# Performance work log

Hardware: AMD Instinct MI355X
Metric: run time of the kernel (lower is better)

## Reference

```python
import jax, jax.numpy as jnp
import numpy as np

B, H, W, C = 32, 64, 64, 192
WS, SHIFT, NH = 8, 4, 6
HID = int(C * 2.0)
N = WS * WS
HD = C // NH
SCALE = HD ** -0.5


def _rel_index():
    coords = np.stack(np.meshgrid(np.arange(WS), np.arange(WS), indexing='ij')).reshape(2, -1)
    rel = (coords[:, :, None] - coords[:, None, :]).transpose(1, 2, 0)
    rel[:, :, 0] += WS - 1
    rel[:, :, 1] += WS - 1
    rel[:, :, 0] *= 2 * WS - 1
    return rel.sum(-1)  # [N, N] int


def _attn_mask():
    img = np.zeros((H, W))
    cnt = 0
    sl = (slice(0, -WS), slice(-WS, -SHIFT), slice(-SHIFT, None))
    for hs in sl:
        for ws_ in sl:
            img[hs, ws_] = cnt
            cnt += 1
    mw = img.reshape(H // WS, WS, W // WS, WS).transpose(0, 2, 1, 3).reshape(-1, N)
    am = mw[:, None, :] - mw[:, :, None]  # unsqueeze(1) - unsqueeze(2)
    return np.where(am != 0, -100.0, 0.0).astype(np.float32)  # [nW, N, N]

REL_IDX = jnp.asarray(_rel_index())
ATTN_MASK = jnp.asarray(_attn_mask())


def _ln(x, g, b, eps=1e-5):
    m = jnp.mean(x, -1, keepdims=True)
    v = jnp.mean((x - m) ** 2, -1, keepdims=True)
    return (x - m) * jax.lax.rsqrt(v + eps) * g + b


def setup_inputs() -> dict:
    key = jax.random.key(0)
    ks = jax.random.split(key, 16)
    s = 0.02
    return {
        'x': jax.random.normal(ks[0], (B, H, W, C), jnp.float32),
        'norm1_g': jnp.ones((C,), jnp.float32),
        'norm1_b': jnp.zeros((C,), jnp.float32),
        'qkv_w': jax.random.normal(ks[1], (C, 3 * C), jnp.float32) * s,
        'qkv_b': jnp.zeros((3 * C,), jnp.float32),
        'proj_w': jax.random.normal(ks[2], (C, C), jnp.float32) * s,
        'proj_b': jnp.zeros((C,), jnp.float32),
        'rel_bias_table': jax.random.normal(ks[3], ((2 * WS - 1) ** 2, NH), jnp.float32) * s,
        'norm2_g': jnp.ones((C,), jnp.float32),
        'norm2_b': jnp.zeros((C,), jnp.float32),
        'mlp_w1': jax.random.normal(ks[4], (C, HID), jnp.float32) * s,
        'mlp_b1': jnp.zeros((HID,), jnp.float32),
        'mlp_w2': jax.random.normal(ks[5], (HID, C), jnp.float32) * s,
        'mlp_b2': jnp.zeros((C,), jnp.float32),
    }


def reference(x, norm1_g, norm1_b, qkv_w, qkv_b, proj_w, proj_b, rel_bias_table,
              norm2_g, norm2_b, mlp_w1, mlp_b1, mlp_w2, mlp_b2):
    nWh, nWw = H // WS, W // WS
    nW = nWh * nWw
    shortcut = x
    h = _ln(x, norm1_g, norm1_b)
    # cyclic shift
    h = jnp.roll(h, shift=(-SHIFT, -SHIFT), axis=(1, 2))
    # window partition -> [B*nW, N, C]
    hw = h.reshape(B, nWh, WS, nWw, WS, C).transpose(0, 1, 3, 2, 4, 5).reshape(B * nW, N, C)
    # qkv
    qkv = hw @ qkv_w + qkv_b  # [B_, N, 3C]
    qkv = qkv.reshape(B * nW, N, 3, NH, HD).transpose(2, 0, 3, 1, 4)
    q, k, v = qkv[0], qkv[1], qkv[2]  # [B_, NH, N, HD]
    attn = jnp.einsum('bhnd,bhmd->bhnm', q * SCALE, k)
    # relative position bias: [NH, N, N]
    bias = rel_bias_table[REL_IDX.reshape(-1)].reshape(N, N, NH).transpose(2, 0, 1)
    attn = attn + bias[None]
    # shift mask
    attn = attn.reshape(B, nW, NH, N, N) + ATTN_MASK[None, :, None]
    attn = jax.nn.softmax(attn.reshape(B * nW, NH, N, N), axis=-1)
    out = jnp.einsum('bhnm,bhmd->bhnd', attn, v).transpose(0, 2, 1, 3).reshape(B * nW, N, C)
    out = out @ proj_w + proj_b
    # window reverse
    out = out.reshape(B, nWh, nWw, WS, WS, C).transpose(0, 1, 3, 2, 4, 5).reshape(B, H, W, C)
    out = jnp.roll(out, shift=(SHIFT, SHIFT), axis=(1, 2))
    h = shortcut + out
    # MLP
    m = _ln(h, norm2_g, norm2_b)
    m = jax.nn.gelu(m @ mlp_w1 + mlp_b1, approximate=False) @ mlp_w2 + mlp_b2
    return h + m
```

## Files before the change

### kernel.cpp

```cpp
#include <hip/hip_runtime.h>
#include <hip/hip_bf16.h>

#define CC 192

typedef __attribute__((ext_vector_type(8))) short bf16x8;
typedef __attribute__((ext_vector_type(4))) float f32x4;

__device__ __forceinline__ unsigned short f2bf(float f) {
    unsigned int u = __float_as_uint(f);
    u = (u + 0x7fffu + ((u >> 16) & 1u)) >> 16;
    return (unsigned short)u;
}

__device__ __forceinline__ float bf2f(unsigned short u) {
    return __uint_as_float(((unsigned int)u) << 16);
}

__device__ __forceinline__ float fast_exp2(float x) {
#if __has_builtin(__builtin_amdgcn_exp2f)
    return __builtin_amdgcn_exp2f(x);
#else
    return __expf(0.69314718055994531f * x);
#endif
}

__device__ __forceinline__ f32x4 mfma16(bf16x8 a, bf16x8 b, f32x4 c) {
    return __builtin_amdgcn_mfma_f32_16x16x32_bf16(a, b, c, 0, 0, 0);
}

__global__ void k_prep(const float* __restrict__ qkv_w, const float* __restrict__ proj_w,
                       const float* __restrict__ w1, const float* __restrict__ w2,
                       const float* __restrict__ relTab,
                       unsigned short* __restrict__ qkvT, unsigned short* __restrict__ projT,
                       unsigned short* __restrict__ w1T, unsigned short* __restrict__ w2T,
                       unsigned short* __restrict__ biasT4) {
    int idx = blockIdx.x * blockDim.x + threadIdx.x;
    if (idx < 110592) { int n = idx / 192, k = idx % 192; qkvT[idx] = f2bf(qkv_w[k * 576 + n]); return; }
    idx -= 110592;
    if (idx < 36864)  { int n = idx / 192, k = idx % 192; projT[idx] = f2bf(proj_w[k * 192 + n]); return; }
    idx -= 36864;
    if (idx < 73728)  { int n = idx / 192, k = idx % 192; w1T[idx] = f2bf(w1[k * 384 + n]); return; }
    idx -= 73728;
    if (idx < 73728)  { int n = idx / 384, k = idx % 384; w2T[idx] = f2bf(w2[k * 192 + n]); return; }
    idx -= 73728;
    if (idx < 98304) {
        const int cls = idx / 24576, rem = idx % 24576;
        const int h = rem >> 12, i = (rem >> 6) & 63, j = rem & 63;
        const int yi = i >> 3, xi = i & 7, yj = j >> 3, xj = j & 7;
        const int rel = (yi - yj + 7) * 15 + (xi - xj + 7);
        float v = relTab[rel * 6 + h];
        const int bH = cls >> 1, bW = cls & 1;
        const int idi = (bH ? (yi >= 4 ? 2 : 1) : 0) * 3 + (bW ? (xi >= 4 ? 2 : 1) : 0);
        const int idj = (bH ? (yj >= 4 ? 2 : 1) : 0) * 3 + (bW ? (xj >= 4 ? 2 : 1) : 0);
        if (idi != idj) v -= 100.f;
        biasT4[idx] = f2bf(v * 1.4426950408889634f);
    }
}

__global__ __launch_bounds__(768, 3) void k_fused(
    const float* __restrict__ x,
    const float* __restrict__ n1g, const float* __restrict__ n1b,
    const unsigned short* __restrict__ qkvT, const float* __restrict__ qkv_b,
    const unsigned short* __restrict__ projT, const float* __restrict__ proj_b,
    const unsigned short* __restrict__ biasT4,
    const float* __restrict__ n2g, const float* __restrict__ n2b,
    const unsigned short* __restrict__ w1T, const float* __restrict__ b1,
    const unsigned short* __restrict__ w2T, const float* __restrict__ b2,
    float* __restrict__ out)
{
    __shared__ __align__(16) char smem[73728];
    __shared__ int sOpos[64];
    char* const rA = smem;
    char* const rQ = smem + 24576;
    char* const rK = smem + 49152;

    const int tid = threadIdx.x;
    const int wid = blockIdx.x;
    const int b = wid >> 6;
    const int win = wid & 63;
    const int wh = win >> 3, ww = win & 7;
    const int lane = tid & 63;
    const int wave = tid >> 6;
    const int lhi = lane >> 4, llo = lane & 15;

    if (tid < 512) {
        const int tok = tid >> 3;
        const int ch0 = (tid & 7) * 24;
        const int yi = tok >> 3, xi = tok & 7;
        const int oy = (wh * 8 + yi + 4) & 63;
        const int ox = (ww * 8 + xi + 4) & 63;
        const int base = ((b * 64 + oy) * 64 + ox) * CC;
        if ((tid & 7) == 0) sOpos[tok] = base;
        float v[24];
        float s = 0.f, ss = 0.f;
        #pragma unroll
        for (int i = 0; i < 6; ++i) {
            const float4 f = *(const float4*)(x + base + ch0 + i * 4);
            v[i*4+0]=f.x; v[i*4+1]=f.y; v[i*4+2]=f.z; v[i*4+3]=f.w;
            s  += f.x + f.y + f.z + f.w;
            ss += f.x*f.x + f.y*f.y + f.z*f.z + f.w*f.w;
        }
        s  += __shfl_xor(s, 1);  s  += __shfl_xor(s, 2);  s  += __shfl_xor(s, 4);
        ss += __shfl_xor(ss, 1); ss += __shfl_xor(ss, 2); ss += __shfl_xor(ss, 4);
        const float mean = s * (1.f / 192.f);
        const float rstd = rsqrtf(ss * (1.f / 192.f) - mean * mean + 1e-5f);
        char* aBase = rA + tok * 384;
        const int sw = (tok & 7) << 4;
        #pragma unroll
        for (int i = 0; i < 12; ++i) {
            const int c = ch0 + i * 2;
            const float a0 = (v[i*2+0] - mean) * rstd * n1g[c]   + n1b[c];
            const float a1 = (v[i*2+1] - mean) * rstd * n1g[c+1] + n1b[c+1];
            *(unsigned int*)(aBase + ((c * 2) ^ sw)) =
                (unsigned int)f2bf(a0) | ((unsigned int)f2bf(a1) << 16);
        }
    }
    __syncthreads();

    {
        const int cbase = wave * 48;
        f32x4 acc[4][3] = {};
        #pragma unroll
        for (int ks = 0; ks < 6; ++ks) {
            bf16x8 af[4];
            const int kbyte = ks * 64 + lhi * 16;
            #pragma unroll
            for (int m = 0; m < 4; ++m) {
                const int row = m * 16 + llo;
                af[m] = *(const bf16x8*)(rA + row * 384 + (kbyte ^ ((row & 7) << 4)));
            }
            #pragma unroll
            for (int n = 0; n < 3; ++n) {
                const int col = cbase + n * 16 + llo;
                const bf16x8 bfr = *(const bf16x8*)(qkvT + col * 192 + ks * 32 + lhi * 8);
                #pragma unroll
                for (int m = 0; m < 4; ++m) acc[m][n] = mfma16(af[m], bfr, acc[m][n]);
            }
        }
        __syncthreads();
        #pragma unroll
        for (int n = 0; n < 3; ++n) {
            const int c0 = cbase + n * 16;
            const int which = c0 / 192;
            const int rem = c0 - which * 192;
            const int h = rem >> 5;
            const int d = (rem & 31) + llo;
            const float bia = qkv_b[c0 + llo];
            #pragma unroll
            for (int m = 0; m < 4; ++m) {
                #pragma unroll
                for (int r = 0; r < 4; ++r) {
                    const int row = m * 16 + lhi * 4 + r;
                    if (which == 0)
                        *(unsigned short*)(rQ + h * 4096 + row * 64 + ((2 * d) ^ ((row & 3) << 4)))
                            = f2bf((acc[m][n][r] + bia) * 0.2550510257216822f);
                    else if (which == 1)
                        *(unsigned short*)(rK + h * 4096 + row * 64 + ((2 * d) ^ ((row & 3) << 4)))
                            = f2bf(acc[m][n][r] + bia);
                    else
                        *(unsigned short*)(rA + h * 4096 + d * 128 + ((2 * row) ^ ((d & 7) << 4)))
                            = f2bf(acc[m][n][r] + bia);
                }
            }
        }
    }
    __syncthreads();

    const int h = wave >> 1;
    const int mh = wave & 1;
    f32x4 pacc[2][2] = {};
    float rinv[2][4];
    {
        bf16x8 qf[2], kf[4];
        #pragma unroll
        for (int m = 0; m < 2; ++m) {
            const int t = (mh * 2 + m) * 16 + llo;
            qf[m] = *(const bf16x8*)(rQ + h * 4096 + t * 64 + ((lhi * 16) ^ ((t & 3) << 4)));
        }
        #pragma unroll
        for (int n = 0; n < 4; ++n) {
            const int t = n * 16 + llo;
            kf[n] = *(const bf16x8*)(rK + h * 4096 + t * 64 + ((lhi * 16) ^ ((t & 3) << 4)));
        }
        __syncthreads();

        f32x4 sacc[2][4] = {};
        #pragma unroll
        for (int m = 0; m < 2; ++m)
            #pragma unroll
            for (int n = 0; n < 4; ++n)
                sacc[m][n] = mfma16(qf[m], kf[n], sacc[m][n]);

        const int cls = ((wh == 7) ? 2 : 0) + ((ww == 7) ? 1 : 0);
        const unsigned short* bT = biasT4 + cls * 24576 + h * 4096;
        #pragma unroll
        for (int m = 0; m < 2; ++m) {
            #pragma unroll
            for (int r = 0; r < 4; ++r) {
                const int i = (mh * 2 + m) * 16 + lhi * 4 + r;
                float sum = 0.f;
                unsigned short pb[4];
                #pragma unroll
                for (int n = 0; n < 4; ++n) {
                    const int j = n * 16 + llo;
                    const float e = fast_exp2(sacc[m][n][r] + bf2f(bT[i * 64 + j]));
                    sum += e;
                    pb[n] = f2bf(e);
                }
                sum += __shfl_xor(sum, 1);
                sum += __shfl_xor(sum, 2);
                sum += __shfl_xor(sum, 4);
                sum += __shfl_xor(sum, 8);
                rinv[m][r] = 1.f / sum;
                #pragma unroll
                for (int n = 0; n < 4; ++n) {
                    const int j = n * 16 + llo;
                    *(unsigned short*)(rQ + h * 8192 + i * 128 + ((2 * j) ^ ((i & 7) << 4))) = pb[n];
                }
            }
        }
        #pragma unroll
        for (int ks = 0; ks < 2; ++ks) {
            bf16x8 pf[2];
            #pragma unroll
            for (int m = 0; m < 2; ++m) {
                const int t = (mh * 2 + m) * 16 + llo;
                pf[m] = *(const bf16x8*)(rQ + h * 8192 + t * 128 + ((ks * 64 + lhi * 16) ^ ((t & 7) << 4)));
            }
            #pragma unroll
            for (int n = 0; n < 2; ++n) {
                const int d = n * 16 + llo;
                const bf16x8 vf = *(const bf16x8*)(rA + h * 4096 + d * 128 + ((ks * 64 + lhi * 16) ^ ((d & 7) << 4)));
                #pragma unroll
                for (int m = 0; m < 2; ++m) pacc[m][n] = mfma16(pf[m], vf, pacc[m][n]);
            }
        }
    }
    __syncthreads();
    {
        #pragma unroll
        for (int m = 0; m < 2; ++m) {
            #pragma unroll
            for (int n = 0; n < 2; ++n) {
                const int c = h * 32 + n * 16 + llo;
                #pragma unroll
                for (int r = 0; r < 4; ++r) {
                    const int i = (mh * 2 + m) * 16 + lhi * 4 + r;
                    *(unsigned short*)(rA + i * 384 + ((c * 2) ^ ((i & 7) << 4)))
                        = f2bf(pacc[m][n][r] * rinv[m][r]);
                }
            }
        }
    }
    __syncthreads();

    {
        const int cbase = wave * 16;
        f32x4 acc[4] = {};
        #pragma unroll
        for (int ks = 0; ks < 6; ++ks) {
            bf16x8 af[4];
            const int kbyte = ks * 64 + lhi * 16;
            #pragma unroll
            for (int m = 0; m < 4; ++m) {
                const int row = m * 16 + llo;
                af[m] = *(const bf16x8*)(rA + row * 384 + (kbyte ^ ((row & 7) << 4)));
            }
            const int col = cbase + llo;
            const bf16x8 bfr = *(const bf16x8*)(projT + col * 192 + ks * 32 + lhi * 8);
            #pragma unroll
            for (int m = 0; m < 4; ++m) acc[m] = mfma16(af[m], bfr, acc[m]);
        }
        const int c = cbase + llo;
        const float pb = proj_b[c];
        #pragma unroll
        for (int m = 0; m < 4; ++m) {
            #pragma unroll
            for (int r = 0; r < 4; ++r) {
                const int i = m * 16 + lhi * 4 + r;
                const float hv = x[sOpos[i] + c] + acc[m][r] + pb;
                *(unsigned short*)(rQ + i * 384 + ((2 * c) ^ ((i & 7) << 4))) = f2bf(hv);
            }
        }
    }
    __syncthreads();

    if (tid < 512) {
        const int tok = tid >> 3;
        const int ch0 = (tid & 7) * 24;
        const int sw = (tok & 7) << 4;
        float v[24]; float s = 0.f, ss = 0.f;
        #pragma unroll
        for (int i = 0; i < 12; ++i) {
            const int c = ch0 + i * 2;
            const unsigned uu = *(const unsigned*)(rQ + tok * 384 + ((2 * c) ^ sw));
            const float a0 = bf2f((unsigned short)uu);
            const float a1 = bf2f((unsigned short)(uu >> 16));
            v[2*i] = a0; v[2*i+1] = a1;
            s += a0 + a1;
            ss += a0 * a0 + a1 * a1;
        }
        s  += __shfl_xor(s, 1);  s  += __shfl_xor(s, 2);  s  += __shfl_xor(s, 4);
        ss += __shfl_xor(ss, 1); ss += __shfl_xor(ss, 2); ss += __shfl_xor(ss, 4);
        const float mean = s * (1.f / 192.f);
        const float rstd = rsqrtf(ss * (1.f / 192.f) - mean * mean + 1e-5f);
        char* aBase = rA + tok * 384;
        #pragma unroll
        for (int i = 0; i < 12; ++i) {
            const int c = ch0 + i * 2;
            const float a0 = (v[i*2]   - mean) * rstd * n2g[c]   + n2b[c];
            const float a1 = (v[i*2+1] - mean) * rstd * n2g[c+1] + n2b[c+1];
            *(unsigned int*)(aBase + ((c * 2) ^ sw)) =
                (unsigned int)f2bf(a0) | ((unsigned int)f2bf(a1) << 16);
        }
    }
    __syncthreads();

    f32x4 accM[4] = {};
    #pragma unroll
    for (int hh = 0; hh < 2; ++hh) {
        {
            f32x4 a1[4] = {};
            #pragma unroll
            for (int ks = 0; ks < 6; ++ks) {
                bf16x8 af[4];
                const int kbyte = ks * 64 + lhi * 16;
                #pragma unroll
                for (int m = 0; m < 4; ++m) {
                    const int row = m * 16 + llo;
                    af[m] = *(const bf16x8*)(rA + row * 384 + (kbyte ^ ((row & 7) << 4)));
                }
                const bf16x8 bfr = *(const bf16x8*)(w1T + (hh * 192 + wave * 16 + llo) * 192 + ks * 32 + lhi * 8);
                #pragma unroll
                for (int m = 0; m < 4; ++m) a1[m] = mfma16(af[m], bfr, a1[m]);
            }
            const int cl = wave * 16 + llo;
            const float bb = b1[hh * 192 + cl];
            #pragma unroll
            for (int m = 0; m < 4; ++m) {
                #pragma unroll
                for (int r = 0; r < 4; ++r) {
                    const int i = m * 16 + lhi * 4 + r;
                    const float u = a1[m][r] + bb;
                    const float xx = 2.3022211096534824f * (u + 0.044715f * u * u * u);
                    const float g = u / (1.f + fast_exp2(-xx));
                    *(unsigned short*)(rK + i * 384 + ((2 * cl) ^ ((i & 7) << 4))) = f2bf(g);
                }
            }
        }
        __syncthreads();
        {
            #pragma unroll
            for (int ks = 0; ks < 6; ++ks) {
                bf16x8 af[4];
                const int kbyte = ks * 64 + lhi * 16;
                #pragma unroll
                for (int m = 0; m < 4; ++m) {
                    const int row = m * 16 + llo;
                    af[m] = *(const bf16x8*)(rK + row * 384 + (kbyte ^ ((row & 7) << 4)));
                }
                const bf16x8 bfr = *(const bf16x8*)(w2T + (wave * 16 + llo) * 384 + hh * 192 + ks * 32 + lhi * 8);
                #pragma unroll
                for (int m = 0; m < 4; ++m) accM[m] = mfma16(af[m], bfr, accM[m]);
            }
        }
        if (hh == 0) __syncthreads();
    }
    {
        const int c = wave * 16 + llo;
        const float bb = b2[c];
        #pragma unroll
        for (int m = 0; m < 4; ++m) {
            #pragma unroll
            for (int r = 0; r < 4; ++r) {
                const int i = m * 16 + lhi * 4 + r;
                const float hv = bf2f(*(const unsigned short*)(rQ + i * 384 + ((2 * c) ^ ((i & 7) << 4))));
                out[sOpos[i] + c] = hv + accM[m][r] + bb;
            }
        }
    }
}

extern "C" void kernel_launch(void* const* d_in, const int* in_sizes, int n_in,
                              void* d_out, int out_size, void* d_ws, size_t ws_size,
                              hipStream_t stream)
{
    const float* x      = (const float*)d_in[0];
    const float* n1g    = (const float*)d_in[1];
    const float* n1b    = (const float*)d_in[2];
    const float* qkv_w  = (const float*)d_in[3];
    const float* qkv_b  = (const float*)d_in[4];
    const float* proj_w = (const float*)d_in[5];
    const float* proj_b = (const float*)d_in[6];
    const float* relTab = (const float*)d_in[7];
    const float* n2g    = (const float*)d_in[8];
    const float* n2b    = (const float*)d_in[9];
    const float* w1     = (const float*)d_in[10];
    const float* b1     = (const float*)d_in[11];
    const float* w2     = (const float*)d_in[12];
    const float* b2     = (const float*)d_in[13];
    float* out = (float*)d_out;

    char* ws = (char*)d_ws;
    unsigned short* qkvT   = (unsigned short*)(ws);
    unsigned short* projT  = (unsigned short*)(ws + 221184);
    unsigned short* w1T    = (unsigned short*)(ws + 294912);
    unsigned short* w2T    = (unsigned short*)(ws + 442368);
    unsigned short* biasT4 = (unsigned short*)(ws + 589824);

    k_prep<<<1536, 256, 0, stream>>>(qkv_w, proj_w, w1, w2, relTab, qkvT, projT, w1T, w2T, biasT4);
    k_fused<<<2048, 768, 0, stream>>>(x, n1g, n1b, qkvT, qkv_b, projT, proj_b, biasT4,
                                      n2g, n2b, w1T, b1, w2T, b2, out);
}
```

Baseline: 277.2 us.

## Use dedicated LDS buffer for P and full MLP hidden to drop barriers

Adds a separate 48KB LDS region so attention probabilities no longer overwrite the Q buffer, which lets one __syncthreads after the Q/K fragment loads be removed. The MLP is restructured so the full 384-wide hidden activation is computed in one pass (each wave now does 32 columns), stored in LDS, then the second GEMM runs over all 12 k-steps with one barrier instead of two half-passes. The bf16 conversion switches to the HIP intrinsic. LDS per block grows from about 72KB to 120KB, which may lower how many 768-thread blocks fit per CU below the launch_bounds target of 3.

Result: no change. 275.0 us (-0.8%).

```diff
diff --git a/kernel.cpp b/kernel.cpp
--- a/kernel.cpp
+++ b/kernel.cpp
@@ -7,9 +7,10 @@
 typedef __attribute__((ext_vector_type(4))) float f32x4;
 
 __device__ __forceinline__ unsigned short f2bf(float f) {
-    unsigned int u = __float_as_uint(f);
-    u = (u + 0x7fffu + ((u >> 16) & 1u)) >> 16;
-    return (unsigned short)u;
+    __hip_bfloat16 h = __float2bfloat16(f);
+    unsigned short u;
+    __builtin_memcpy(&u, &h, 2);
+    return u;
 }
 
 __device__ __forceinline__ float bf2f(unsigned short u) {
@@ -68,11 +69,12 @@
     const unsigned short* __restrict__ w2T, const float* __restrict__ b2,
     float* __restrict__ out)
 {
-    __shared__ __align__(16) char smem[73728];
+    __shared__ __align__(16) char smem[122880];
     __shared__ int sOpos[64];
     char* const rA = smem;
     char* const rQ = smem + 24576;
     char* const rK = smem + 49152;
+    char* const rP = smem + 73728;
 
     const int tid = threadIdx.x;
     const int wid = blockIdx.x;
@@ -131,8 +133,7 @@
             }
             #pragma unroll
             for (int n = 0; n < 3; ++n) {
-                const int col = cbase + n * 16 + llo;
-                const bf16x8 bfr = *(const bf16x8*)(qkvT + col * 192 + ks * 32 + lhi * 8);
+                const bf16x8 bfr = *(const bf16x8*)(qkvT + (cbase + n * 16 + llo) * 192 + ks * 32 + lhi * 8);
                 #pragma unroll
                 for (int m = 0; m < 4; ++m) acc[m][n] = mfma16(af[m], bfr, acc[m][n]);
             }
@@ -182,7 +183,6 @@
             const int t = n * 16 + llo;
             kf[n] = *(const bf16x8*)(rK + h * 4096 + t * 64 + ((lhi * 16) ^ ((t & 3) << 4)));
         }
-        __syncthreads();
 
         f32x4 sacc[2][4] = {};
         #pragma unroll
@@ -193,6 +193,7 @@
 
         const int cls = ((wh == 7) ? 2 : 0) + ((ww == 7) ? 1 : 0);
         const unsigned short* bT = biasT4 + cls * 24576 + h * 4096;
+        char* const pBase = rP + h * 8192;
         #pragma unroll
         for (int m = 0; m < 2; ++m) {
             #pragma unroll
@@ -215,7 +216,7 @@
                 #pragma unroll
                 for (int n = 0; n < 4; ++n) {
                     const int j = n * 16 + llo;
-                    *(unsigned short*)(rQ + h * 8192 + i * 128 + ((2 * j) ^ ((i & 7) << 4))) = pb[n];
+                    *(unsigned short*)(pBase + i * 128 + ((2 * j) ^ ((i & 7) << 4))) = pb[n];
                 }
             }
         }
@@ -225,7 +226,7 @@
             #pragma unroll
             for (int m = 0; m < 2; ++m) {
                 const int t = (mh * 2 + m) * 16 + llo;
-                pf[m] = *(const bf16x8*)(rQ + h * 8192 + t * 128 + ((ks * 64 + lhi * 16) ^ ((t & 7) << 4)));
+                pf[m] = *(const bf16x8*)(pBase + t * 128 + ((ks * 64 + lhi * 16) ^ ((t & 7) << 4)));
             }
             #pragma unroll
             for (int n = 0; n < 2; ++n) {
@@ -266,8 +267,7 @@
                 const int row = m * 16 + llo;
                 af[m] = *(const bf16x8*)(rA + row * 384 + (kbyte ^ ((row & 7) << 4)));
             }
-            const int col = cbase + llo;
-            const bf16x8 bfr = *(const bf16x8*)(projT + col * 192 + ks * 32 + lhi * 8);
+            const bf16x8 bfr = *(const bf16x8*)(projT + (cbase + llo) * 192 + ks * 32 + lhi * 8);
             #pragma unroll
             for (int m = 0; m < 4; ++m) acc[m] = mfma16(af[m], bfr, acc[m]);
         }
@@ -316,58 +316,60 @@
     }
     __syncthreads();
 
-    f32x4 accM[4] = {};
-    #pragma unroll
-    for (int hh = 0; hh < 2; ++hh) {
-        {
-            f32x4 a1[4] = {};
-            #pragma unroll
-            for (int ks = 0; ks < 6; ++ks) {
-                bf16x8 af[4];
-                const int kbyte = ks * 64 + lhi * 16;
-                #pragma unroll
-                for (int m = 0; m < 4; ++m) {
-                    const int row = m * 16 + llo;
-                    af[m] = *(const bf16x8*)(rA + row * 384 + (kbyte ^ ((row & 7) << 4)));
-                }
-                const bf16x8 bfr = *(const bf16x8*)(w1T + (hh * 192 + wave * 16 + llo) * 192 + ks * 32 + lhi * 8);
-                #pragma unroll
-                for (int m = 0; m < 4; ++m) a1[m] = mfma16(af[m], bfr, a1[m]);
-            }
-            const int cl = wave * 16 + llo;
-            const float bb = b1[hh * 192 + cl];
+    {
+        const int cbase = wave * 32;
+        f32x4 a1[4][2] = {};
+        #pragma unroll
+        for (int ks = 0; ks < 6; ++ks) {
+            bf16x8 af[4];
+            const int kbyte = ks * 64 + lhi * 16;
+            #pragma unroll
+            for (int m = 0; m < 4; ++m) {
+                const int row = m * 16 + llo;
+                af[m] = *(const bf16x8*)(rA + row * 384 + (kbyte ^ ((row & 7) << 4)));
+            }
+            #pragma unroll
+            for (int n = 0; n < 2; ++n) {
+                const bf16x8 bfr = *(const bf16x8*)(w1T + (cbase + n * 16 + llo) * 192 + ks * 32 + lhi * 8);
+                #pragma unroll
+                for (int m = 0; m < 4; ++m) a1[m][n] = mfma16(af[m], bfr, a1[m][n]);
+            }
+        }
+        #pragma unroll
+        for (int n = 0; n < 2; ++n) {
+            const int c = cbase + n * 16 + llo;
+            const float bb = b1[c];
             #pragma unroll
             for (int m = 0; m < 4; ++m) {
                 #pragma unroll
                 for (int r = 0; r < 4; ++r) {
                     const int i = m * 16 + lhi * 4 + r;
-                    const float u = a1[m][r] + bb;
+                    const float u = a1[m][n][r] + bb;
                     const float xx = 2.3022211096534824f * (u + 0.044715f * u * u * u);
                     const float g = u / (1.f + fast_exp2(-xx));
-                    *(unsigned short*)(rK + i * 384 + ((2 * cl) ^ ((i & 7) << 4))) = f2bf(g);
+                    *(unsigned short*)(rP + i * 768 + ((2 * c) ^ ((i & 7) << 4))) = f2bf(g);
                 }
             }
         }
-        __syncthreads();
-        {
-            #pragma unroll
-            for (int ks = 0; ks < 6; ++ks) {
-                bf16x8 af[4];
-                const int kbyte = ks * 64 + lhi * 16;
-                #pragma unroll
-                for (int m = 0; m < 4; ++m) {
-                    const int row = m * 16 + llo;
-                    af[m] = *(const bf16x8*)(rK + row * 384 + (kbyte ^ ((row & 7) << 4)));
-                }
-                const bf16x8 bfr = *(const bf16x8*)(w2T + (wave * 16 + llo) * 384 + hh * 192 + ks * 32 + lhi * 8);
-                #pragma unroll
-                for (int m = 0; m < 4; ++m) accM[m] = mfma16(af[m], bfr, accM[m]);
-            }
-        }
-        if (hh == 0) __syncthreads();
-    }
+    }
+    __syncthreads();
+
     {
         const int c = wave * 16 + llo;
+        f32x4 accM[4] = {};
+        #pragma unroll
+        for (int ks = 0; ks < 12; ++ks) {
+            bf16x8 af[4];
+            const int kbyte = ks * 64 + lhi * 16;
+            #pragma unroll
+            for (int m = 0; m < 4; ++m) {
+                const int row = m * 16 + llo;
+                af[m] = *(const bf16x8*)(rP + row * 768 + (kbyte ^ ((row & 7) << 4)));
+            }
+            const bf16x8 bfr = *(const bf16x8*)(w2T + c * 384 + ks * 32 + lhi * 8);
+            #pragma unroll
+            for (int m = 0; m < 4; ++m) accM[m] = mfma16(af[m], bfr, accM[m]);
+        }
         const float bb = b2[c];
         #pragma unroll
         for (int m = 0; m < 4; ++m) {
```
